# Performance work log

Hardware: AMD Instinct MI355X
Metric: run time of the kernel (lower is better)

The kernel has to match this reference:

```python
import jax, jax.numpy as jnp
import numpy as np
import math

R_ON = 0.05
ALPHA = 0.001  # training-mode alpha (module zeroes it only in eval)


def _fmod(a, b):
    # b/pi * atan(tan(pi*(a/b - 0.5))) + b/2, as in the torch source
    return b / math.pi * jnp.arctan(jnp.tan(math.pi * (a / b - 0.5))) + b / 2


def setup_inputs() -> dict:
    key = jax.random.key(0)
    ks = jax.random.split(key, 7)
    B, T, H = 64, 512, 768
    stdv = 1.0 / math.sqrt(H)
    x = jax.random.normal(ks[0], (B, T, H), dtype=jnp.float32)
    W = jax.random.uniform(ks[1], (4 * H, 4 * H), minval=-stdv, maxval=stdv, dtype=jnp.float32)
    U = jax.random.uniform(ks[2], (4 * H, 4 * H), minval=-stdv, maxval=stdv, dtype=jnp.float32)
    b = jnp.zeros((4 * H,), dtype=jnp.float32)
    w_peep = jax.random.uniform(ks[3], (3 * H,), minval=-stdv, maxval=stdv, dtype=jnp.float32)
    tau = jnp.exp(jax.random.uniform(ks[4], (H,), minval=0.0, maxval=3.0, dtype=jnp.float32))
    shift = jax.random.uniform(ks[5], (H,), minval=0.0, maxval=float(jnp.mean(tau)), dtype=jnp.float32)
    return {"x": x, "W": W, "U": U, "b": b, "w_peep": w_peep, "tau": tau, "shift": shift}


def reference(x, W, U, b, w_peep, tau, shift):
    B, T, H = x.shape
    # x_t.repeat(1,3) @ W[:3H,:3H] == x_t @ (W[:H,:3H] + W[H:2H,:3H] + W[2H:3H,:3H])
    W3 = W[:3 * H, :3 * H]
    U3 = U[:3 * H, :3 * H]
    Wsum = W3[:H] + W3[H:2 * H] + W3[2 * H:3 * H]  # (H, 3H)
    Usum = U3[:H] + U3[H:2 * H] + U3[2 * H:3 * H]  # (H, 3H)
    b3 = b[:3 * H]
    Wc = W[3 * H:4 * H, 3 * H:4 * H]
    Uc = U[3 * H:4 * H, 3 * H:4 * H]
    bc = b[3 * H:4 * H]

    # Phase gate k[t,h]
    times = jnp.arange(T, dtype=jnp.float32)[:, None]  # (T,1) broadcast to (T,H)
    phi = _fmod(times - shift, tau) / (tau + 1e-8)
    k = jnp.where(
        phi < 0.5 * R_ON,
        2.0 * phi / R_ON,
        jnp.where((0.5 * R_ON <= phi) & (phi < R_ON), 2.0 - 2.0 * phi / R_ON, ALPHA * phi),
    )  # (T, H)

    h0 = jnp.zeros((B, H), dtype=x.dtype)
    c0 = jnp.zeros((B, H), dtype=x.dtype)

    def step(carry, inp):
        h, c = carry
        x_t, k_t = inp  # (B,H), (H,)
        c3 = jnp.tile(c, (1, 3))
        gates = x_t @ Wsum + h @ Usum + b3 + w_peep * c3  # (B, 3H)
        i_t = jax.nn.sigmoid(gates[:, :H])
        f_t = jax.nn.sigmoid(gates[:, H:2 * H])
        o_t = jax.nn.sigmoid(gates[:, 2 * H:3 * H])
        gate_c = x_t @ Wc + h @ Uc + bc
        c_prim = f_t * c + i_t * jnp.tanh(gate_c)
        c_new = k_t * c_prim + (1.0 - k_t) * c
        h_prim = jnp.tanh(c_prim) * o_t
        h_new = k_t * h_prim + (1.0 - k_t) * h
        return (h_new, c_new), h_new

    xs = (jnp.transpose(x, (1, 0, 2)), k)  # time-major
    _, h_out = jax.lax.scan(step, (h0, c0), xs)
    return jnp.transpose(h_out, (1, 0, 2))  # (B, T, H)
```

## Files before the change

### kernel.cpp

```cpp
#include <hip/hip_runtime.h>
#include <math.h>


#define HDIM 768
#define BDIM 64
#define TDIM 512
#define G_BLOCKS 96
#define ND 8

typedef float f32x4 __attribute__((ext_vector_type(4)));
typedef float f32x2 __attribute__((ext_vector_type(2)));
typedef __bf16 bf16x8 __attribute__((ext_vector_type(8)));
typedef _Float16 f16x2 __attribute__((ext_vector_type(2)));
typedef int i32x4 __attribute__((ext_vector_type(4)));
typedef int i32x2 __attribute__((ext_vector_type(2)));

#define OFF_FLAGS 0
#define OFF_HBUF0 24576
#define OFF_HBUF1 (24576 + 98304)
#define OFF_KTAB  (24576 + 2*98304)
#define OFF_WT    (OFF_KTAB + (size_t)512*768*4)
#define OFF_XB    (OFF_WT + (size_t)3072*1536*2)
#define WS_NEED_FULL (OFF_XB + (size_t)512*64*768*2)
#define OFF_GX    OFF_XB
#define WS_NEED_GXF32 (OFF_GX + (size_t)32768*3072*4)
#define WS_NEED_GXF16 (OFF_GX + (size_t)32768*3072*2)


__global__ void k_wcomb(const float* __restrict__ W, const float* __restrict__ U,
                        __bf16* __restrict__ WT) {
  __shared__ __bf16 tile[32][33];
  int tk = blockIdx.x % 48;
  int tn = blockIdx.x / 48;
  int tx = threadIdx.x & 31, ty = threadIdx.x >> 5;
  int k0 = tk * 32, n0 = tn * 32;
#pragma unroll
  for (int i = 0; i < 4; ++i) {
    int k = k0 + ty + 8 * i;
    int n = n0 + tx;
    const float* M = (k < 768) ? W : U;
    int r = (k < 768) ? k : k - 768;
    float v;
    if (n < 2304)
      v = M[(size_t)r * 3072 + n] + M[(size_t)(768 + r) * 3072 + n] +
          M[(size_t)(1536 + r) * 3072 + n];
    else
      v = M[(size_t)(2304 + r) * 3072 + n];
    tile[ty + 8 * i][tx] = (__bf16)v;
  }
  __syncthreads();
#pragma unroll
  for (int i = 0; i < 4; ++i) {
    int n = n0 + ty + 8 * i;
    int k = k0 + tx;
    WT[(size_t)n * 1536 + k] = tile[tx][ty + 8 * i];
  }
}

__global__ void k_ktab(const float* __restrict__ tau, const float* __restrict__ shift,
                       float* __restrict__ kT) {
  int idx = blockIdx.x * 256 + threadIdx.x;
  int d = idx % 768, t = idx / 768;
  float bb = tau[d];
  float a = (float)t - shift[d];
  const float PI = 3.14159265358979323846f;
  float fm = bb / PI * atanf(tanf(PI * (a / bb - 0.5f))) + bb * 0.5f;
  float phi = fm / (bb + 1e-8f);
  float kv;
  if (phi < 0.5f * 0.05f)      kv = 2.0f * phi / 0.05f;
  else if (phi < 0.05f)        kv = 2.0f - 2.0f * phi / 0.05f;
  else                         kv = 0.001f * phi;
  kT[idx] = kv;
}

__global__ void k_xb(const float* __restrict__ x, __bf16* __restrict__ xb) {
  int idx = blockIdx.x * 256 + threadIdx.x;
  int k = idx % 768;
  int tb = idx / 768;
  int b = tb % 64, t = tb / 64;
  xb[idx] = (__bf16)x[((size_t)b * 512 + t) * 768 + k];
}

template <int F16OUT>
__global__ __launch_bounds__(256, 2)
void k_xgemm(const float* __restrict__ x, const __bf16* __restrict__ Wt,
             void* __restrict__ Cv) {
  __shared__ __align__(16) unsigned char AsB[128 * 128];
  __shared__ __align__(16) unsigned char BsB[128 * 128];
  const int tid = threadIdx.x;
  const int wave = tid >> 6, lane = tid & 63;
  const int quad = lane >> 4, l15 = lane & 15;
  const int wr = wave >> 1, wc = wave & 1;
  const int mt = blockIdx.x / 24, nt = blockIdx.x % 24;
  const int m0 = mt * 128, n0 = nt * 128;

  f32x4 acc[4][4];
#pragma unroll
  for (int i = 0; i < 4; ++i)
#pragma unroll
    for (int jj = 0; jj < 4; ++jj) acc[i][jj] = (f32x4){0.f, 0.f, 0.f, 0.f};

  for (int kt = 0; kt < 12; ++kt) {
#pragma unroll
    for (int s0 = 0; s0 < 4; ++s0) {
      int s = s0 * 256 + tid;
      int row = s >> 3, part = s & 7;
      int sw = (row & 7) << 4;
      int m = m0 + row;
      const float* ap = x + ((size_t)(m & 63) * 512 + (m >> 6)) * 768 + kt * 64 + part * 8;
      f32x4 a0 = *(const f32x4*)ap;
      f32x4 a1 = *(const f32x4*)(ap + 4);
      bf16x8 av;
#pragma unroll
      for (int q = 0; q < 4; ++q) { av[q] = (__bf16)a0[q]; av[q + 4] = (__bf16)a1[q]; }
      *(bf16x8*)&AsB[row * 128 + ((part * 16) ^ sw)] = av;
      i32x4 vb = *(const i32x4*)((const unsigned char*)Wt +
                                 (size_t)(n0 + row) * 3072 + kt * 128 + part * 16);
      *(i32x4*)&BsB[row * 128 + ((part * 16) ^ sw)] = vb;
    }
    __syncthreads();
#pragma unroll
    for (int ks = 0; ks < 2; ++ks) {
      const int cb = (ks * 32 + quad * 8) * 2;
      bf16x8 af[4], bfr[4];
#pragma unroll
      for (int f = 0; f < 4; ++f) {
        int ar = wr * 64 + f * 16 + l15;
        af[f] = *(const bf16x8*)&AsB[ar * 128 + (cb ^ ((ar & 7) << 4))];
        int br = wc * 64 + f * 16 + l15;
        bfr[f] = *(const bf16x8*)&BsB[br * 128 + (cb ^ ((br & 7) << 4))];
      }
#pragma unroll
      for (int fm = 0; fm < 4; ++fm)
#pragma unroll
        for (int fn = 0; fn < 4; ++fn)
          acc[fm][fn] = __builtin_amdgcn_mfma_f32_16x16x32_bf16(af[fm], bfr[fn],
                                                                acc[fm][fn], 0, 0, 0);
    }
    __syncthreads();
  }
#pragma unroll
  for (int fm = 0; fm < 4; ++fm) {
    int m = m0 + wr * 64 + fm * 16 + quad * 4;
#pragma unroll
    for (int fn = 0; fn < 4; ++fn) {
      int n = n0 + wc * 64 + fn * 16 + l15;
#pragma unroll
      for (int r = 0; r < 4; ++r) {
        if constexpr (F16OUT)
          ((_Float16*)Cv)[(size_t)(m + r) * 3072 + n] = (_Float16)acc[fm][fn][r];
        else
          ((float*)Cv)[(size_t)(m + r) * 3072 + n] = acc[fm][fn][r];
      }
    }
  }
}

__device__ __forceinline__ i32x4 ldg_c16(const void* p) {
  i32x4 r;
  asm volatile("global_load_dwordx4 %0, %1, off sc0 sc1" : "=v"(r) : "v"(p));
  return r;
}
__device__ __forceinline__ i32x2 ldg_n8(const void* p) {
  i32x2 r;
  asm volatile("global_load_dwordx2 %0, %1, off" : "=v"(r) : "v"(p));
  return r;
}
__device__ __forceinline__ int ldg_n4(const void* p) {
  int r;
  asm volatile("global_load_dword %0, %1, off" : "=v"(r) : "v"(p));
  return r;
}
__device__ __forceinline__ void stg_c4(void* p, int v) {
  asm volatile("global_store_dword %0, %1, off sc0 sc1"
               :: "v"(p), "v"(v) : "memory");
}
__device__ __forceinline__ void stg_n8(void* p, i32x2 v) {
  asm volatile("global_store_dwordx2 %0, %1, off"
               :: "v"(p), "v"(v) : "memory");
}
__device__ __forceinline__ void waitcnt_vm0() {
  asm volatile("s_waitcnt vmcnt(0)" ::: "memory");
}
__device__ __forceinline__ void ldg_c4_pair_nowait(const void* a, const void* b,
                                                   int& r0, int& r1) {
  asm volatile("global_load_dword %0, %2, off sc0 sc1\n\t"
               "global_load_dword %1, %3, off sc0 sc1"
               : "=v"(r0), "=v"(r1) : "v"(a), "v"(b) : "memory");
}
__device__ __forceinline__ void waitcnt_vm0_pin2(int& a, int& b) {
  asm volatile("s_waitcnt vmcnt(0)" : "+v"(a), "+v"(b) :: "memory");
}
#define HOLD4(x) asm volatile("" : "+v"(x))
#define HOLD2(x) asm volatile("" : "+v"(x))
#define HOLDI(x) asm volatile("" : "+v"(x))

__device__ __forceinline__ float sigm_f(float x) {
  return __fdividef(1.f, 1.f + __expf(-x));
}
__device__ __forceinline__ float tanh_f(float x) {
  return 1.f - __fdividef(2.f, __expf(2.f * x) + 1.f);
}

#define HSTEP(i, VMS)                                                         \
  asm volatile("s_waitcnt vmcnt(" VMS ")");                                   \
  HOLD4(hr[i][0]); HOLD4(hr[i][1]); HOLD4(hr[i][2]); HOLD4(hr[i][3]);         \
  { const int kc = 96 + (wave * 6 + (i)) * 4 + quad;                          \
    bf16x8 b0 = *(const bf16x8*)&Bl2[(size_t)(kc * 32 + l15) * 8];            \
    bf16x8 b1 = *(const bf16x8*)&Bl2[(size_t)(kc * 32 + 16 + l15) * 8];       \
    _Pragma("unroll")                                                         \
    for (int rt = 0; rt < 4; ++rt) {                                          \
      bf16x8 av = __builtin_bit_cast(bf16x8, hr[i][rt]);                      \
      acc[rt][0] = __builtin_amdgcn_mfma_f32_16x16x32_bf16(av, b0, acc[rt][0], 0, 0, 0); \
      acc[rt][1] = __builtin_amdgcn_mfma_f32_16x16x32_bf16(av, b1, acc[rt][1], 0, 0, 0); \
    } }

template <int MODE>
__global__ __launch_bounds__(256, 1)
void k_lstm(const __bf16* __restrict__ xb, const float* __restrict__ xf,
            const void* __restrict__ gxv,
            const __bf16* __restrict__ WT, const float* __restrict__ kT,
            const float* __restrict__ bias, const float* __restrict__ wpeep,
            __bf16* h0buf, __bf16* h1buf, float* __restrict__ out, int* flags) {
  const int j = blockIdx.x, d0 = j * ND;
  const int tid = threadIdx.x;
  const int wave = tid >> 6, lane = tid & 63;
  const int quad = lane >> 4, l15 = lane & 15;

  __shared__ __align__(16) __bf16 Bl2[192 * 32 * 8];
  __shared__ float gacc2[4][32][68];

  for (int idx = tid + (MODE >= 2 ? 3072 : 0); idx < 6144; idx += 256) {
    int c = idx & 31, kc = idx >> 5;
    int n = (c >> 3) * 768 + d0 + (c & 7);
    *(bf16x8*)&Bl2[(size_t)idx * 8] = *(const bf16x8*)&WT[(size_t)n * 1536 + kc * 8];
  }

  const int dq = tid & 3, bb = tid >> 2;
  const int ed0 = d0 + dq * 2;
  const f32x2 bi2  = *(const f32x2*)&bias[ed0];
  const f32x2 bf2  = *(const f32x2*)&bias[768 + ed0];
  const f32x2 bo2  = *(const f32x2*)&bias[1536 + ed0];
  const f32x2 bc2  = *(const f32x2*)&bias[2304 + ed0];
  const f32x2 wpi2 = *(const f32x2*)&wpeep[ed0];
  const f32x2 wpf2 = *(const f32x2*)&wpeep[768 + ed0];
  const f32x2 wpo2 = *(const f32x2*)&wpeep[1536 + ed0];

  const int fid0 = wave * 96 + lane;
  const int fid1 = wave * 96 + 64 + (lane & 31);
  const int* fp0 = flags + fid0 * 16;
  const int* fp1 = flags + fid1 * 16;

  f32x2 creg; creg[0] = 0.f; creg[1] = 0.f;
  f32x2 hreg; hreg[0] = 0.f; hreg[1] = 0.f;

  int ready = 0;

  __syncthreads();

  for (int t = 0; t < TDIM; ++t) {
    const __bf16* hcur = (t & 1) ? h1buf : h0buf;
    __bf16* hnxt = (t & 1) ? h0buf : h1buf;

    f32x4 acc[4][2];
#pragma unroll
    for (int rt = 0; rt < 4; ++rt) {
      acc[rt][0] = (f32x4){0.f, 0.f, 0.f, 0.f};
      acc[rt][1] = (f32x4){0.f, 0.f, 0.f, 0.f};
    }

    if constexpr (MODE < 2) {
#pragma unroll
      for (int i = 0; i < 6; ++i) {
        const int kk = (wave * 6 + i) * 32 + quad * 8;
        const int kc = kk >> 3;
        bf16x8 a[4];
        if constexpr (MODE == 1) {
#pragma unroll
          for (int rt = 0; rt < 4; ++rt)
            a[rt] = *(const bf16x8*)(xb + ((size_t)(t * 64 + rt * 16 + l15)) * 768 + kk);
        } else {
#pragma unroll
          for (int rt = 0; rt < 4; ++rt)
#pragma unroll
            for (int q = 0; q < 8; ++q)
              a[rt][q] = (__bf16)xf[((size_t)(rt * 16 + l15) * 512 + t) * 768 + kk + q];
        }
        bf16x8 b0 = *(const bf16x8*)&Bl2[(size_t)(kc * 32 + l15) * 8];
        bf16x8 b1 = *(const bf16x8*)&Bl2[(size_t)(kc * 32 + 16 + l15) * 8];
#pragma unroll
        for (int rt = 0; rt < 4; ++rt) {
          acc[rt][0] = __builtin_amdgcn_mfma_f32_16x16x32_bf16(a[rt], b0, acc[rt][0], 0, 0, 0);
          acc[rt][1] = __builtin_amdgcn_mfma_f32_16x16x32_bf16(a[rt], b1, acc[rt][1], 0, 0, 0);
        }
      }
    }

    if (MODE < 2 || !ready) {
      for (;;) {
        int v0, v1;
        asm volatile("global_load_dword %0, %2, off sc0 sc1\n\t"
                     "global_load_dword %1, %3, off sc0 sc1\n\t"
                     "s_waitcnt vmcnt(0)"
                     : "=v"(v0), "=v"(v1) : "v"(fp0), "v"(fp1) : "memory");
        if (__all(v0 >= t && v1 >= t)) break;
        __builtin_amdgcn_s_sleep(1);
      }
    }

    i32x2 ktraw = ldg_n8(kT + (size_t)t * 768 + ed0);
    i32x2 gx8[4];
    int   gx4[4];
    if constexpr (MODE == 2) {
#pragma unroll
      for (int g = 0; g < 4; ++g)
        gx8[g] = ldg_n8((const float*)gxv + ((size_t)(t * 64 + bb)) * 3072 + g * 768 + ed0);
    } else if constexpr (MODE == 3) {
#pragma unroll
      for (int g = 0; g < 4; ++g)
        gx4[g] = ldg_n4((const _Float16*)gxv + ((size_t)(t * 64 + bb)) * 3072 + g * 768 + ed0);
    }

    i32x4 hr[6][4];
#pragma unroll
    for (int i = 0; i < 6; ++i) {
      const int hoff = (wave * 6 + i) * 32 + quad * 8;
#pragma unroll
      for (int rt = 0; rt < 4; ++rt)
        hr[i][rt] = ldg_c16(hcur + (size_t)(rt * 16 + l15) * 768 + hoff);
    }
    HSTEP(0, "20")
    HSTEP(1, "16")
    HSTEP(2, "12")
    HSTEP(3, "8")
    HSTEP(4, "4")
    HSTEP(5, "0")
    HOLD2(ktraw);
    if constexpr (MODE == 2) { HOLD2(gx8[0]); HOLD2(gx8[1]); HOLD2(gx8[2]); HOLD2(gx8[3]); }
    if constexpr (MODE == 3) { HOLDI(gx4[0]); HOLDI(gx4[1]); HOLDI(gx4[2]); HOLDI(gx4[3]); }

#pragma unroll
    for (int rt = 0; rt < 4; ++rt) {
      *(f32x4*)&gacc2[wave][l15][rt * 16 + quad * 4]      = acc[rt][0];
      *(f32x4*)&gacc2[wave][16 + l15][rt * 16 + quad * 4] = acc[rt][1];
    }
    __syncthreads();

    f32x2 kt2 = __builtin_bit_cast(f32x2, ktraw);
    float gs[2][4];
#pragma unroll
    for (int dd = 0; dd < 2; ++dd)
#pragma unroll
      for (int g = 0; g < 4; ++g) {
        float s = 0.f;
#pragma unroll
        for (int w = 0; w < 4; ++w) s += gacc2[w][g * 8 + dq * 2 + dd][bb];
        if constexpr (MODE == 2)
          s += __builtin_bit_cast(f32x2, gx8[g])[dd];
        if constexpr (MODE == 3)
          s += (float)__builtin_bit_cast(f16x2, gx4[g])[dd];
        gs[dd][g] = s;
      }
    __syncthreads();

    f32x2 cnv, hnv;
#pragma unroll
    for (int dd = 0; dd < 2; ++dd) {
      float c_prev = creg[dd], h_prev = hreg[dd], kt = kt2[dd];
      float gi = gs[dd][0] + bi2[dd] + wpi2[dd] * c_prev;
      float gf = gs[dd][1] + bf2[dd] + wpf2[dd] * c_prev;
      float go = gs[dd][2] + bo2[dd] + wpo2[dd] * c_prev;
      float gc = gs[dd][3] + bc2[dd];
      float iv = sigm_f(gi);
      float fv = sigm_f(gf);
      float ov = sigm_f(go);
      float cp = fv * c_prev + iv * tanh_f(gc);
      float cn = kt * cp + (1.f - kt) * c_prev;
      float hp = tanh_f(cp) * ov;
      float hn = kt * hp + (1.f - kt) * h_prev;
      cnv[dd] = cn; hnv[dd] = hn;
    }
    creg = cnv; hreg = hnv;

    __bf16 h0 = (__bf16)hnv[0], h1 = (__bf16)hnv[1];
    unsigned hu = (unsigned)__builtin_bit_cast(unsigned short, h0) |
                  ((unsigned)__builtin_bit_cast(unsigned short, h1) << 16);
    stg_c4(hnxt + (size_t)bb * 768 + ed0, (int)hu);
    f32x2 ov2; ov2[0] = hnv[0]; ov2[1] = hnv[1];
    stg_n8(out + ((size_t)bb * 512 + t) * 768 + ed0, __builtin_bit_cast(i32x2, ov2));
    if constexpr (MODE >= 2) {
      int p0, p1;
      ldg_c4_pair_nowait(fp0, fp1, p0, p1);
      waitcnt_vm0_pin2(p0, p1);
      if (lane == 0) stg_c4(flags + (j * 4 + wave) * 16, t + 1);
      ready = __all(p0 >= t + 1 && p1 >= t + 1);
    } else {
      waitcnt_vm0();
      if (lane == 0) stg_c4(flags + (j * 4 + wave) * 16, t + 1);
    }
  }
}

extern "C" void kernel_launch(void* const* d_in, const int* in_sizes, int n_in,
                              void* d_out, int out_size, void* d_ws, size_t ws_size,
                              hipStream_t stream) {
  const float* x     = (const float*)d_in[0];
  const float* W     = (const float*)d_in[1];
  const float* U     = (const float*)d_in[2];
  const float* bias  = (const float*)d_in[3];
  const float* wpeep = (const float*)d_in[4];
  const float* tau   = (const float*)d_in[5];
  const float* shift = (const float*)d_in[6];
  float* out = (float*)d_out;
  char* ws = (char*)d_ws;

  int*    flags = (int*)(ws + OFF_FLAGS);
  __bf16* hb0 = (__bf16*)(ws + OFF_HBUF0);
  __bf16* hb1 = (__bf16*)(ws + OFF_HBUF1);
  float*  kT  = (float*)(ws + OFF_KTAB);
  __bf16* WT  = (__bf16*)(ws + OFF_WT);
  __bf16* xb  = (__bf16*)(ws + OFF_XB);
  void*   gxp = (void*)(ws + OFF_GX);

  int mode;
  if      (ws_size >= WS_NEED_GXF32) mode = 2;
  else if (ws_size >= WS_NEED_GXF16) mode = 3;
  else if (ws_size >= WS_NEED_FULL)  mode = 1;
  else                               mode = 0;

  hipMemsetAsync(ws, 0, OFF_KTAB, stream);
  k_wcomb<<<48 * 96, 256, 0, stream>>>(W, U, WT);
  k_ktab<<<(512 * 768) / 256, 256, 0, stream>>>(tau, shift, kT);

  if (mode == 2) {
    k_xgemm<0><<<256 * 24, 256, 0, stream>>>(x, WT, gxp);
    k_lstm<2><<<G_BLOCKS, 256, 0, stream>>>(nullptr, x, gxp, WT, kT, bias, wpeep,
                                            hb0, hb1, out, flags);
  } else if (mode == 3) {
    k_xgemm<1><<<256 * 24, 256, 0, stream>>>(x, WT, gxp);
    k_lstm<3><<<G_BLOCKS, 256, 0, stream>>>(nullptr, x, gxp, WT, kT, bias, wpeep,
                                            hb0, hb1, out, flags);
  } else if (mode == 1) {
    k_xb<<<(512 * 64 * 768) / 256, 256, 0, stream>>>(x, xb);
    k_lstm<1><<<G_BLOCKS, 256, 0, stream>>>(xb, x, nullptr, WT, kT, bias, wpeep,
                                            hb0, hb1, out, flags);
  } else {
    k_lstm<0><<<G_BLOCKS, 256, 0, stream>>>(nullptr, x, nullptr, WT, kT, bias, wpeep,
                                            hb0, hb1, out, flags);
  }
}
```

Measured before the change: 4.079 ms.

## Embed timestep tags in h buffer to replace flag polling synchronization

Switches the inter-block handshake in the precomputed-gates modes. Each bf16 pair of h is now stored with a timestep tag in an 8-byte unit, and consumers poll the h data itself until every tag matches the step, so the separate flag barrier and its extra round trip drop out. The poll is split into two halves so MFMA work on the first half can overlap loading the second. In exchange the h buffers double in size, every poll moves twice the bytes, and a spin limit marks a block dead if the tags never arrive.

```diff
diff --git a/kernel.cpp b/kernel.cpp
--- a/kernel.cpp
+++ b/kernel.cpp
@@ -17,8 +17,8 @@
 
 #define OFF_FLAGS 0
 #define OFF_HBUF0 24576
-#define OFF_HBUF1 (24576 + 98304)
-#define OFF_KTAB  (24576 + 2*98304)
+#define OFF_HBUF1 (24576 + 196608)
+#define OFF_KTAB  (24576 + 2*196608)
 #define OFF_WT    (OFF_KTAB + (size_t)512*768*4)
 #define OFF_XB    (OFF_WT + (size_t)3072*1536*2)
 #define WS_NEED_FULL (OFF_XB + (size_t)512*64*768*2)
@@ -175,6 +175,10 @@
   asm volatile("global_store_dword %0, %1, off sc0 sc1"
                :: "v"(p), "v"(v) : "memory");
 }
+__device__ __forceinline__ void stg_c8(void* p, i32x2 v) {
+  asm volatile("global_store_dwordx2 %0, %1, off sc0 sc1"
+               :: "v"(p), "v"(v) : "memory");
+}
 __device__ __forceinline__ void stg_n8(void* p, i32x2 v) {
   asm volatile("global_store_dwordx2 %0, %1, off"
                :: "v"(p), "v"(v) : "memory");
@@ -182,15 +186,6 @@
 __device__ __forceinline__ void waitcnt_vm0() {
   asm volatile("s_waitcnt vmcnt(0)" ::: "memory");
 }
-__device__ __forceinline__ void ldg_c4_pair_nowait(const void* a, const void* b,
-                                                   int& r0, int& r1) {
-  asm volatile("global_load_dword %0, %2, off sc0 sc1\n\t"
-               "global_load_dword %1, %3, off sc0 sc1"
-               : "=v"(r0), "=v"(r1) : "v"(a), "v"(b) : "memory");
-}
-__device__ __forceinline__ void waitcnt_vm0_pin2(int& a, int& b) {
-  asm volatile("s_waitcnt vmcnt(0)" : "+v"(a), "+v"(b) :: "memory");
-}
 #define HOLD4(x) asm volatile("" : "+v"(x))
 #define HOLD2(x) asm volatile("" : "+v"(x))
 #define HOLDI(x) asm volatile("" : "+v"(x))
@@ -201,6 +196,43 @@
 __device__ __forceinline__ float tanh_f(float x) {
   return 1.f - __fdividef(2.f, __expf(2.f * x) + 1.f);
 }
+
+#define TPOLL(ha, I0)                                                          \
+  if (!dead) {                                                                 \
+    int spins = 0;                                                             \
+    for (;;) {                                                                 \
+      _Pragma("unroll") for (int ii = 0; ii < 3; ++ii)                         \
+        _Pragma("unroll") for (int rt = 0; rt < 4; ++rt)                       \
+          _Pragma("unroll") for (int u = 0; u < 2; ++u)                        \
+            ha[ii][rt][u] = ldg_c16(hb + (size_t)((rt * 16 + l15) * 384 +      \
+                             (wave * 6 + (I0) + ii) * 16 + quad * 4 + u * 2) * 8);\
+      waitcnt_vm0();                                                           \
+      int okv = 1;                                                             \
+      _Pragma("unroll") for (int ii = 0; ii < 3; ++ii)                         \
+        _Pragma("unroll") for (int rt = 0; rt < 4; ++rt)                       \
+          _Pragma("unroll") for (int u = 0; u < 2; ++u) {                      \
+            HOLD4(ha[ii][rt][u]);                                              \
+            okv &= (ha[ii][rt][u][1] == t) & (ha[ii][rt][u][3] == t);          \
+          }                                                                    \
+      if (__all(okv)) break;                                                   \
+      if (++spins > (1 << 20)) { dead = 1; break; }                            \
+      __builtin_amdgcn_s_sleep(1);                                             \
+    }                                                                          \
+  }
+
+#define TMFMA(ha, I0)                                                          \
+  _Pragma("unroll") for (int ii = 0; ii < 3; ++ii) {                           \
+    const int kc = 96 + (wave * 6 + (I0) + ii) * 4 + quad;                     \
+    bf16x8 b0 = *(const bf16x8*)&Bl2[(size_t)(kc * 32 + l15) * 8];             \
+    bf16x8 b1 = *(const bf16x8*)&Bl2[(size_t)(kc * 32 + 16 + l15) * 8];        \
+    _Pragma("unroll") for (int rt = 0; rt < 4; ++rt) {                         \
+      i32x4 dv;                                                                \
+      dv[0] = ha[ii][rt][0][0]; dv[1] = ha[ii][rt][0][2];                      \
+      dv[2] = ha[ii][rt][1][0]; dv[3] = ha[ii][rt][1][2];                      \
+      bf16x8 av = __builtin_bit_cast(bf16x8, dv);                              \
+      acc[rt][0] = __builtin_amdgcn_mfma_f32_16x16x32_bf16(av, b0, acc[rt][0], 0, 0, 0); \
+      acc[rt][1] = __builtin_amdgcn_mfma_f32_16x16x32_bf16(av, b1, acc[rt][1], 0, 0, 0); \
+    } }
 
 #define HSTEP(i, VMS)                                                         \
   asm volatile("s_waitcnt vmcnt(" VMS ")");                                   \
@@ -221,7 +253,7 @@
             const void* __restrict__ gxv,
             const __bf16* __restrict__ WT, const float* __restrict__ kT,
             const float* __restrict__ bias, const float* __restrict__ wpeep,
-            __bf16* h0buf, __bf16* h1buf, float* __restrict__ out, int* flags) {
+            void* h0buf, void* h1buf, float* __restrict__ out, int* flags) {
   const int j = blockIdx.x, d0 = j * ND;
   const int tid = threadIdx.x;
   const int wave = tid >> 6, lane = tid & 63;
@@ -254,14 +286,11 @@
   f32x2 creg; creg[0] = 0.f; creg[1] = 0.f;
   f32x2 hreg; hreg[0] = 0.f; hreg[1] = 0.f;
 
-  int ready = 0;
+  int dead = 0;
 
   __syncthreads();
 
   for (int t = 0; t < TDIM; ++t) {
-    const __bf16* hcur = (t & 1) ? h1buf : h0buf;
-    __bf16* hnxt = (t & 1) ? h0buf : h1buf;
-
     f32x4 acc[4][2];
 #pragma unroll
     for (int rt = 0; rt < 4; ++rt) {
@@ -269,7 +298,86 @@
       acc[rt][1] = (f32x4){0.f, 0.f, 0.f, 0.f};
     }
 
-    if constexpr (MODE < 2) {
+    i32x2 ktraw = ldg_n8(kT + (size_t)t * 768 + ed0);
+    i32x2 gx8[4];
+    int   gx4[4];
+    if constexpr (MODE == 2) {
+#pragma unroll
+      for (int g = 0; g < 4; ++g)
+        gx8[g] = ldg_n8((const float*)gxv + ((size_t)(t * 64 + bb)) * 3072 + g * 768 + ed0);
+    } else if constexpr (MODE == 3) {
+#pragma unroll
+      for (int g = 0; g < 4; ++g)
+        gx4[g] = ldg_n4((const _Float16*)gxv + ((size_t)(t * 64 + bb)) * 3072 + g * 768 + ed0);
+    }
+
+    if constexpr (MODE >= 2) {
+      const char* hb = (const char*)((t & 1) ? h1buf : h0buf);
+      char*       hn = (char*)((t & 1) ? h0buf : h1buf);
+
+      i32x4 ha[3][4][2];
+      TPOLL(ha, 0)
+      HOLD2(ktraw);
+      if constexpr (MODE == 2) { HOLD2(gx8[0]); HOLD2(gx8[1]); HOLD2(gx8[2]); HOLD2(gx8[3]); }
+      if constexpr (MODE == 3) { HOLDI(gx4[0]); HOLDI(gx4[1]); HOLDI(gx4[2]); HOLDI(gx4[3]); }
+      TMFMA(ha, 0)
+      TPOLL(ha, 3)
+      TMFMA(ha, 3)
+
+#pragma unroll
+      for (int rt = 0; rt < 4; ++rt) {
+        *(f32x4*)&gacc2[wave][l15][rt * 16 + quad * 4]      = acc[rt][0];
+        *(f32x4*)&gacc2[wave][16 + l15][rt * 16 + quad * 4] = acc[rt][1];
+      }
+      __syncthreads();
+
+      f32x2 kt2 = __builtin_bit_cast(f32x2, ktraw);
+      float gs[2][4];
+#pragma unroll
+      for (int dd = 0; dd < 2; ++dd)
+#pragma unroll
+        for (int g = 0; g < 4; ++g) {
+          float s = 0.f;
+#pragma unroll
+          for (int w = 0; w < 4; ++w) s += gacc2[w][g * 8 + dq * 2 + dd][bb];
+          if constexpr (MODE == 2)
+            s += __builtin_bit_cast(f32x2, gx8[g])[dd];
+          else
+            s += (float)__builtin_bit_cast(f16x2, gx4[g])[dd];
+          gs[dd][g] = s;
+        }
+      __syncthreads();
+
+      f32x2 cnv, hnv;
+#pragma unroll
+      for (int dd = 0; dd < 2; ++dd) {
+        float c_prev = creg[dd], h_prev = hreg[dd], kt = kt2[dd];
+        float gi = gs[dd][0] + bi2[dd] + wpi2[dd] * c_prev;
+        float gf = gs[dd][1] + bf2[dd] + wpf2[dd] * c_prev;
+        float go = gs[dd][2] + bo2[dd] + wpo2[dd] * c_prev;
+        float gc = gs[dd][3] + bc2[dd];
+        float iv = sigm_f(gi);
+        float fv = sigm_f(gf);
+        float ov = sigm_f(go);
+        float cp = fv * c_prev + iv * tanh_f(gc);
+        float cn = kt * cp + (1.f - kt) * c_prev;
+        float hp = tanh_f(cp) * ov;
+        float hn2 = kt * hp + (1.f - kt) * h_prev;
+        cnv[dd] = cn; hnv[dd] = hn2;
+      }
+      creg = cnv; hreg = hnv;
+
+      __bf16 h0 = (__bf16)hnv[0], h1 = (__bf16)hnv[1];
+      unsigned hu = (unsigned)__builtin_bit_cast(unsigned short, h0) |
+                    ((unsigned)__builtin_bit_cast(unsigned short, h1) << 16);
+      i32x2 unit; unit[0] = (int)hu; unit[1] = t + 1;
+      stg_c8(hn + (size_t)(bb * 384 + j * 4 + dq) * 8, unit);
+      f32x2 ov2; ov2[0] = hnv[0]; ov2[1] = hnv[1];
+      stg_n8(out + ((size_t)bb * 512 + t) * 768 + ed0, __builtin_bit_cast(i32x2, ov2));
+    } else {
+      const __bf16* hcur = (const __bf16*)((t & 1) ? h1buf : h0buf);
+      __bf16* hnxt = (__bf16*)((t & 1) ? h0buf : h1buf);
+
 #pragma unroll
       for (int i = 0; i < 6; ++i) {
         const int kk = (wave * 6 + i) * 32 + quad * 8;
@@ -294,9 +402,7 @@
           acc[rt][1] = __builtin_amdgcn_mfma_f32_16x16x32_bf16(a[rt], b1, acc[rt][1], 0, 0, 0);
         }
       }
-    }
-
-    if (MODE < 2 || !ready) {
+
       for (;;) {
         int v0, v1;
         asm volatile("global_load_dword %0, %2, off sc0 sc1\n\t"
@@ -306,97 +412,70 @@
         if (__all(v0 >= t && v1 >= t)) break;
         __builtin_amdgcn_s_sleep(1);
       }
-    }
-
-    i32x2 ktraw = ldg_n8(kT + (size_t)t * 768 + ed0);
-    i32x2 gx8[4];
-    int   gx4[4];
-    if constexpr (MODE == 2) {
-#pragma unroll
-      for (int g = 0; g < 4; ++g)
-        gx8[g] = ldg_n8((const float*)gxv + ((size_t)(t * 64 + bb)) * 3072 + g * 768 + ed0);
-    } else if constexpr (MODE == 3) {
-#pragma unroll
-      for (int g = 0; g < 4; ++g)
-        gx4[g] = ldg_n4((const _Float16*)gxv + ((size_t)(t * 64 + bb)) * 3072 + g * 768 + ed0);
-    }
-
-    i32x4 hr[6][4];
-#pragma unroll
-    for (int i = 0; i < 6; ++i) {
-      const int hoff = (wave * 6 + i) * 32 + quad * 8;
-#pragma unroll
-      for (int rt = 0; rt < 4; ++rt)
-        hr[i][rt] = ldg_c16(hcur + (size_t)(rt * 16 + l15) * 768 + hoff);
-    }
-    HSTEP(0, "20")
-    HSTEP(1, "16")
-    HSTEP(2, "12")
-    HSTEP(3, "8")
-    HSTEP(4, "4")
-    HSTEP(5, "0")
-    HOLD2(ktraw);
-    if constexpr (MODE == 2) { HOLD2(gx8[0]); HOLD2(gx8[1]); HOLD2(gx8[2]); HOLD2(gx8[3]); }
-    if constexpr (MODE == 3) { HOLDI(gx4[0]); HOLDI(gx4[1]); HOLDI(gx4[2]); HOLDI(gx4[3]); }
-
-#pragma unroll
-    for (int rt = 0; rt < 4; ++rt) {
-      *(f32x4*)&gacc2[wave][l15][rt * 16 + quad * 4]      = acc[rt][0];
-      *(f32x4*)&gacc2[wave][16 + l15][rt * 16 + quad * 4] = acc[rt][1];
-    }
-    __syncthreads();
-
-    f32x2 kt2 = __builtin_bit_cast(f32x2, ktraw);
-    float gs[2][4];
-#pragma unroll
-    for (int dd = 0; dd < 2; ++dd)
-#pragma unroll
-      for (int g = 0; g < 4; ++g) {
-        float s = 0.f;
-#pragma unroll
-        for (int w = 0; w < 4; ++w) s += gacc2[w][g * 8 + dq * 2 + dd][bb];
-        if constexpr (MODE == 2)
-          s += __builtin_bit_cast(f32x2, gx8[g])[dd];
-        if constexpr (MODE == 3)
-          s += (float)__builtin_bit_cast(f16x2, gx4[g])[dd];
-        gs[dd][g] = s;
-      }
-    __syncthreads();
-
-    f32x2 cnv, hnv;
-#pragma unroll
-    for (int dd = 0; dd < 2; ++dd) {
-      float c_prev = creg[dd], h_prev = hreg[dd], kt = kt2[dd];
-      float gi = gs[dd][0] + bi2[dd] + wpi2[dd] * c_prev;
-      float gf = gs[dd][1] + bf2[dd] + wpf2[dd] * c_prev;
-      float go = gs[dd][2] + bo2[dd] + wpo2[dd] * c_prev;
-      float gc = gs[dd][3] + bc2[dd];
-      float iv = sigm_f(gi);
-      float fv = sigm_f(gf);
-      float ov = sigm_f(go);
-      float cp = fv * c_prev + iv * tanh_f(gc);
-      float cn = kt * cp + (1.f - kt) * c_prev;
-      float hp = tanh_f(cp) * ov;
-      float hn = kt * hp + (1.f - kt) * h_prev;
-      cnv[dd] = cn; hnv[dd] = hn;
-    }
-    creg = cnv; hreg = hnv;
-
-    __bf16 h0 = (__bf16)hnv[0], h1 = (__bf16)hnv[1];
-    unsigned hu = (unsigned)__builtin_bit_cast(unsigned short, h0) |
-                  ((unsigned)__builtin_bit_cast(unsigned short, h1) << 16);
-    stg_c4(hnxt + (size_t)bb * 768 + ed0, (int)hu);
-    f32x2 ov2; ov2[0] = hnv[0]; ov2[1] = hnv[1];
-    stg_n8(out + ((size_t)bb * 512 + t) * 768 + ed0, __builtin_bit_cast(i32x2, ov2));
-    if constexpr (MODE >= 2) {
-      int p0, p1;
-      ldg_c4_pair_nowait(fp0, fp1, p0, p1);
-      waitcnt_vm0_pin2(p0, p1);
-      if (lane == 0) stg_c4(flags + (j * 4 + wave) * 16, t + 1);
-      ready = __all(p0 >= t + 1 && p1 >= t + 1);
-    } else {
+      HOLD2(ktraw);
+
+      i32x4 hr[6][4];
+#pragma unroll
+      for (int i = 0; i < 6; ++i) {
+        const int hoff = (wave * 6 + i) * 32 + quad * 8;
+#pragma unroll
+        for (int rt = 0; rt < 4; ++rt)
+          hr[i][rt] = ldg_c16(hcur + (size_t)(rt * 16 + l15) * 768 + hoff);
+      }
+      HSTEP(0, "20")
+      HSTEP(1, "16")
+      HSTEP(2, "12")
+      HSTEP(3, "8")
+      HSTEP(4, "4")
+      HSTEP(5, "0")
+
+#pragma unroll
+      for (int rt = 0; rt < 4; ++rt) {
+        *(f32x4*)&gacc2[wave][l15][rt * 16 + quad * 4]      = acc[rt][0];
+        *(f32x4*)&gacc2[wave][16 + l15][rt * 16 + quad * 4] = acc[rt][1];
+      }
+      __syncthreads();
+
+      f32x2 kt2 = __builtin_bit_cast(f32x2, ktraw);
+      float gs[2][4];
+#pragma unroll
+      for (int dd = 0; dd < 2; ++dd)
+#pragma unroll
+        for (int g = 0; g < 4; ++g) {
+          float s = 0.f;
+#pragma unroll
+          for (int w = 0; w < 4; ++w) s += gacc2[w][g * 8 + dq * 2 + dd][bb];
+          gs[dd][g] = s;
+        }
+      __syncthreads();
+
+      f32x2 cnv, hnv;
+#pragma unroll
+      for (int dd = 0; dd < 2; ++dd) {
+        float c_prev = creg[dd], h_prev = hreg[dd], kt = kt2[dd];
+        float gi = gs[dd][0] + bi2[dd] + wpi2[dd] * c_prev;
+        float gf = gs[dd][1] + bf2[dd] + wpf2[dd] * c_prev;
+        float go = gs[dd][2] + bo2[dd] + wpo2[dd] * c_prev;
+        float gc = gs[dd][3] + bc2[dd];
+        float iv = sigm_f(gi);
+        float fv = sigm_f(gf);
+        float ov = sigm_f(go);
+        float cp = fv * c_prev + iv * tanh_f(gc);
+        float cn = kt * cp + (1.f - kt) * c_prev;
+        float hp = tanh_f(cp) * ov;
+        float hn2 = kt * hp + (1.f - kt) * h_prev;
+        cnv[dd] = cn; hnv[dd] = hn2;
+      }
+      creg = cnv; hreg = hnv;
+
+      __bf16 h0 = (__bf16)hnv[0], h1 = (__bf16)hnv[1];
+      unsigned hu = (unsigned)__builtin_bit_cast(unsigned short, h0) |
+                    ((unsigned)__builtin_bit_cast(unsigned short, h1) << 16);
+      stg_c4(hnxt + (size_t)bb * 768 + ed0, (int)hu);
       waitcnt_vm0();
       if (lane == 0) stg_c4(flags + (j * 4 + wave) * 16, t + 1);
+      f32x2 ov2; ov2[0] = hnv[0]; ov2[1] = hnv[1];
+      stg_n8(out + ((size_t)bb * 512 + t) * 768 + ed0, __builtin_bit_cast(i32x2, ov2));
     }
   }
 }
@@ -415,8 +494,8 @@
   char* ws = (char*)d_ws;
 
   int*    flags = (int*)(ws + OFF_FLAGS);
-  __bf16* hb0 = (__bf16*)(ws + OFF_HBUF0);
-  __bf16* hb1 = (__bf16*)(ws + OFF_HBUF1);
+  void*   hb0 = (void*)(ws + OFF_HBUF0);
+  void*   hb1 = (void*)(ws + OFF_HBUF1);
   float*  kT  = (float*)(ws + OFF_KTAB);
   __bf16* WT  = (__bf16*)(ws + OFF_WT);
   __bf16* xb  = (__bf16*)(ws + OFF_XB);
```

After: 5.049 ms. 1.24x slower.
